# Optimization experiments

Measured on AMD Instinct MI355X. Metric: run time of the kernel, lower is better.

Reference implementation:

```python
import jax, jax.numpy as jnp
import numpy as np

B = 8
H1c = W1c = 56
H2c = W2c = 112
C1 = 512
C2 = 256
NH = 8
WS = 7
POOL = 2
EPS = 1e-5


def setup_inputs() -> dict:
    key = jax.random.key(0)
    ks = jax.random.split(key, 8)
    x = jax.random.normal(ks[0], (B, H1c * W1c, C1), dtype=jnp.float32)
    y = jax.random.normal(ks[1], (B, H2c * W2c, C2), dtype=jnp.float32)
    Wq = jax.random.normal(ks[2], (C1, C1), dtype=jnp.float32) * 0.02
    Wkv = jax.random.normal(ks[3], (2 * C1, C2), dtype=jnp.float32) * 0.02
    Wproj = jax.random.normal(ks[4], (C1, C1), dtype=jnp.float32) * 0.02
    bproj = jnp.zeros((C1,), dtype=jnp.float32)
    # 1x1 conv: fan_out = out_channels -> std = sqrt(2/C2)
    Wsr = jax.random.normal(ks[5], (C2, C2), dtype=jnp.float32) * np.sqrt(2.0 / C2).astype(np.float32)
    bsr = jnp.zeros((C2,), dtype=jnp.float32)
    gn = jnp.ones((C2,), dtype=jnp.float32)
    bn = jnp.zeros((C2,), dtype=jnp.float32)
    return {"x": x, "y": y, "Wq": Wq, "Wkv": Wkv, "Wproj": Wproj,
            "bproj": bproj, "Wsr": Wsr, "bsr": bsr, "gn": gn, "bn": bn,
            "H1": H1c, "W1": W1c, "H2": H2c, "W2": W2c}


def _window_partition(t, ws):
    # t: (B, nh, H, W, C) -> (B*nh, num_windows, ws*ws, C)
    Bt, n, H, W, C = t.shape
    ht, wt = H // ws, W // ws
    t = t.reshape(Bt, n, ht, ws, wt, ws, C).transpose(0, 1, 2, 4, 3, 5, 6)
    return t.reshape(Bt * n, ht * wt, ws * ws, C)


def reference(x, y, Wq, Wkv, Wproj, bproj, Wsr, bsr, gn, bn, H1, W1, H2, W2):
    B1, N1, c1 = x.shape
    B2, N2, c2 = y.shape
    nh, ws = NH, WS
    hd = c1 // nh
    scale = hd ** (-0.5)

    # q projection -> (B, nh, H1, W1, hd)
    q = (x @ Wq.T).reshape(B1, H1, W1, nh, hd).transpose(0, 3, 1, 2, 4)

    # KV preprocessing: avgpool -> 1x1 conv -> layernorm -> gelu
    y2 = y.transpose(0, 2, 1).reshape(B2, c2, H2, W2)
    Hp, Wp = H2 // POOL, W2 // POOL
    y2 = y2.reshape(B2, c2, Hp, POOL, Wp, POOL).mean(axis=(3, 5))
    y2 = jnp.einsum('bchw,oc->bohw', y2, Wsr) + bsr[None, :, None, None]
    y2 = y2.reshape(B2, c2, Hp * Wp).transpose(0, 2, 1)  # (B, Np, C2)
    mu = y2.mean(-1, keepdims=True)
    var = y2.var(-1, keepdims=True)
    y2 = (y2 - mu) / jnp.sqrt(var + EPS) * gn + bn
    y2 = jax.nn.gelu(y2, approximate=False)

    kv = (y2 @ Wkv.T).reshape(B2, Hp * Wp, 2, nh, hd)
    k = kv[:, :, 0].transpose(0, 2, 1, 3).reshape(B2, nh, Hp, Wp, hd)
    v = kv[:, :, 1].transpose(0, 2, 1, 3).reshape(B2, nh, Hp, Wp, hd)

    qw = _window_partition(q, ws)   # (B*nh, nw, ws^2, hd)
    kw = _window_partition(k, ws)
    vw = _window_partition(v, ws)

    attn = jax.nn.softmax(jnp.einsum('bnqd,bnkd->bnqk', qw, kw) * scale, axis=-1)
    out = jnp.einsum('bnqk,bnkd->bnqd', attn, vw)  # (B*nh, nw, ws^2, hd)

    # window reverse -> (B, N1, C1)
    ht, wt = H1 // ws, W1 // ws
    out = out.reshape(B1, nh, ht, wt, ws, ws, hd).transpose(0, 1, 2, 4, 3, 5, 6)
    out = out.reshape(B1, nh, H1 * W1, hd).transpose(0, 2, 1, 3).reshape(B1, H1 * W1, c1)
    return out @ Wproj.T + bproj
```

## Files before the change

kernel.cpp:

```cpp
#include <hip/hip_runtime.h>
#include <hip/hip_bf16.h>

typedef __attribute__((ext_vector_type(8))) short short8;
typedef __attribute__((ext_vector_type(4))) float f32x4;
typedef __attribute__((ext_vector_type(4))) unsigned short ushort4v;

#define DI __device__ __forceinline__

DI unsigned short f2bf(float f) {
  union { float f; unsigned int u; } a; a.f = f;
  unsigned int u = a.u;
  return (unsigned short)((u + 0x7FFFu + ((u >> 16) & 1u)) >> 16);
}

#define BARRIER() do { asm volatile("" ::: "memory"); __builtin_amdgcn_s_barrier(); asm volatile("" ::: "memory"); } while (0)
#define GLOAD16(src, dst) __builtin_amdgcn_global_load_lds( \
    (const __attribute__((address_space(1))) void*)(src), \
    (__attribute__((address_space(3))) void*)(dst), 16, 0, 0)


__global__ __launch_bounds__(256)
void cvt_pool(const float* __restrict__ y, unsigned short* __restrict__ pooled,
              const float* __restrict__ Wq, const float* __restrict__ Wsr,
              const float* __restrict__ Wkv, const float* __restrict__ Wproj,
              unsigned short* __restrict__ Wq_b, unsigned short* __restrict__ Wsr_b,
              unsigned short* __restrict__ WkvF, unsigned short* __restrict__ WprojF) {
  int bid = blockIdx.x;
  int tid = threadIdx.x;
  if (bid < 6272) {
    int t = bid * 256 + tid;
    int cv = (t & 63) * 4;
    int bp = t >> 6;
    int b = bp / 3136, p = bp % 3136;
    int hp = p / 56, wp = p % 56;
    const float* src = y + (((size_t)b * 12544) + hp * 224 + wp * 2) * 256 + cv;
    float4 a0 = *(const float4*)(src);
    float4 a1 = *(const float4*)(src + 256);
    float4 a2 = *(const float4*)(src + 28672);
    float4 a3 = *(const float4*)(src + 28672 + 256);
    float4 av;
    av.x = (a0.x + a1.x + a2.x + a3.x) * 0.25f;
    av.y = (a0.y + a1.y + a2.y + a3.y) * 0.25f;
    av.z = (a0.z + a1.z + a2.z + a3.z) * 0.25f;
    av.w = (a0.w + a1.w + a2.w + a3.w) * 0.25f;
    ushort4v o = { f2bf(av.x), f2bf(av.y), f2bf(av.z), f2bf(av.w) };
    *(ushort4v*)&pooled[(size_t)bp * 256 + cv] = o;
  } else if (bid < 6592) {
    const float* src; unsigned short* dst; long off;
    if (bid < 6528) { src = Wq;  dst = Wq_b;  off = (long)(bid - 6272) * 1024 + tid * 4; }
    else            { src = Wsr; dst = Wsr_b; off = (long)(bid - 6528) * 1024 + tid * 4; }
    float4 v = *(const float4*)&src[off];
    ushort4v o = { f2bf(v.x), f2bf(v.y), f2bf(v.z), f2bf(v.w) };
    *(ushort4v*)&dst[off] = o;
  } else if (bid < 6720) {
    int t = (bid - 6592) * 4 + (tid >> 6);
    int lane = tid & 63, lr = lane & 15, lg = lane >> 4;
    int ks = t & 1, kt = (t >> 1) & 3, nf2 = (t >> 3) & 1;
    int half = (t >> 4) & 1, head = (t >> 5) & 7, h2 = (t >> 8) & 1;
    int row = h2 * 512 + head * 64 + half * 32 + nf2 * 16 + lr;
    int col = kt * 64 + (ks * 4 + lg) * 8;
    const float* s = Wkv + (size_t)row * 256 + col;
    float4 v0 = *(const float4*)s, v1 = *(const float4*)(s + 4);
    union { short8 sv; unsigned short u[8]; } w;
    w.u[0] = f2bf(v0.x); w.u[1] = f2bf(v0.y); w.u[2] = f2bf(v0.z); w.u[3] = f2bf(v0.w);
    w.u[4] = f2bf(v1.x); w.u[5] = f2bf(v1.y); w.u[6] = f2bf(v1.z); w.u[7] = f2bf(v1.w);
    *(short8*)&WkvF[((size_t)t << 9) + lane * 8] = w.sv;
  } else {
    int t = (bid - 6720) * 4 + (tid >> 6);
    int lane = tid & 63, lr = lane & 15, lg = lane >> 4;
    int ks = t & 1, kt = (t >> 1) & 7, nf = (t >> 4) & 3, head = (t >> 6) & 7;
    int row = head * 64 + nf * 16 + lr;
    int col = kt * 64 + (ks * 4 + lg) * 8;
    const float* s = Wproj + (size_t)row * 512 + col;
    float4 v0 = *(const float4*)s, v1 = *(const float4*)(s + 4);
    union { short8 sv; unsigned short u[8]; } w;
    w.u[0] = f2bf(v0.x); w.u[1] = f2bf(v0.y); w.u[2] = f2bf(v0.z); w.u[3] = f2bf(v0.w);
    w.u[4] = f2bf(v1.x); w.u[5] = f2bf(v1.y); w.u[6] = f2bf(v1.z); w.u[7] = f2bf(v1.w);
    *(short8*)&WprojF[((size_t)t << 9) + lane * 8] = w.sv;
  }
}

__global__ __launch_bounds__(256)
void sr_gemm(const unsigned short* __restrict__ Ap, const unsigned short* __restrict__ Wsr_b,
             const float* __restrict__ bsr, const float* __restrict__ gn,
             const float* __restrict__ bn, unsigned short* __restrict__ out) {
  __shared__ unsigned short sA[64 * 64];
  __shared__ unsigned short sB[256 * 64];
  __shared__ float red[64 * 8];

  const int tid = threadIdx.x;
  const int wv = tid >> 6;
  const int lane = tid & 63;
  const int lr = lane & 15;
  const int lg = lane >> 4;
  const int lr4 = lg * 4;
  const int m0 = blockIdx.x * 64;
  const int sr8 = lane >> 3;
  const int sl8 = lane & 7;

  f32x4 acc[4][4];
#pragma unroll
  for (int i = 0; i < 4; ++i)
#pragma unroll
    for (int j = 0; j < 4; ++j) acc[i][j] = (f32x4){0.f, 0.f, 0.f, 0.f};

  for (int kt = 0; kt < 256; kt += 64) {
#pragma unroll
    for (int c = 0; c < 2; ++c) {
      int row = wv * 16 + c * 8 + sr8;
      GLOAD16(Ap + (size_t)(m0 + row) * 256 + kt + ((sl8 ^ (row & 7)) * 8),
              &sA[(wv * 16 + c * 8) * 64]);
    }
#pragma unroll
    for (int c = 0; c < 8; ++c) {
      int row = wv * 64 + c * 8 + sr8;
      GLOAD16(Wsr_b + (size_t)row * 256 + kt + ((sl8 ^ (row & 7)) * 8),
              &sB[(wv * 64 + c * 8) * 64]);
    }
    __syncthreads();
#pragma unroll
    for (int ks = 0; ks < 2; ++ks) {
      short8 af[4], bfr[4];
#pragma unroll
      for (int i = 0; i < 4; ++i)
        af[i] = *(const short8*)&sA[(i * 16 + lr) * 64 + (((ks * 4 + lg) ^ (lr & 7)) * 8)];
#pragma unroll
      for (int j = 0; j < 4; ++j)
        bfr[j] = *(const short8*)&sB[(wv * 64 + j * 16 + lr) * 64 + (((ks * 4 + lg) ^ (lr & 7)) * 8)];
#pragma unroll
      for (int i = 0; i < 4; ++i)
#pragma unroll
        for (int j = 0; j < 4; ++j)
          acc[i][j] = __builtin_amdgcn_mfma_f32_16x16x32_bf16(af[i], bfr[j], acc[i][j], 0, 0, 0);
    }
    __syncthreads();
  }

  float bsv[4], gnv[4], bnv[4];
#pragma unroll
  for (int j = 0; j < 4; ++j) {
    int col = wv * 64 + j * 16 + lr;
    bsv[j] = bsr[col]; gnv[j] = gn[col]; bnv[j] = bn[col];
  }
  float s_[4][4], q_[4][4];
#pragma unroll
  for (int i = 0; i < 4; ++i)
#pragma unroll
    for (int r = 0; r < 4; ++r) {
      float s = 0.f, q = 0.f;
#pragma unroll
      for (int j = 0; j < 4; ++j) {
        float v = acc[i][j][r] + bsv[j];
        acc[i][j][r] = v;
        s += v; q += v * v;
      }
      s_[i][r] = s; q_[i][r] = q;
    }
#pragma unroll
  for (int m = 1; m <= 8; m <<= 1)
#pragma unroll
    for (int i = 0; i < 4; ++i)
#pragma unroll
      for (int r = 0; r < 4; ++r) {
        s_[i][r] += __shfl_xor(s_[i][r], m);
        q_[i][r] += __shfl_xor(q_[i][r], m);
      }
  if (lr == 0) {
#pragma unroll
    for (int i = 0; i < 4; ++i)
#pragma unroll
      for (int r = 0; r < 4; ++r) {
        int row = i * 16 + lr4 + r;
        red[row * 8 + wv * 2 + 0] = s_[i][r];
        red[row * 8 + wv * 2 + 1] = q_[i][r];
      }
  }
  __syncthreads();
#pragma unroll
  for (int i = 0; i < 4; ++i) {
#pragma unroll
    for (int r = 0; r < 4; ++r) {
      int row = i * 16 + lr4 + r;
      float sum = red[row * 8 + 0] + red[row * 8 + 2] + red[row * 8 + 4] + red[row * 8 + 6];
      float sq  = red[row * 8 + 1] + red[row * 8 + 3] + red[row * 8 + 5] + red[row * 8 + 7];
      float mean = sum * (1.f / 256.f);
      float var = sq * (1.f / 256.f) - mean * mean;
      float rstd = rsqrtf(var + 1e-5f);
#pragma unroll
      for (int j = 0; j < 4; ++j) {
        float t = (acc[i][j][r] - mean) * rstd * gnv[j] + bnv[j];
        t = 0.5f * t * (1.f + erff(t * 0.70710678118654752f));
        out[(size_t)(m0 + row) * 256 + wv * 64 + j * 16 + lr] = f2bf(t);
      }
    }
  }
}

DI void epi_q(int gm, int gc, float v, unsigned short* outp) {
  const int b = gm / 3136, pos = gm % 3136;
  const int h = pos / 56, ww = pos % 56;
  const int head = gc >> 6, d = gc & 63;
  const size_t idx = ((((size_t)(b * 8 + head)) * 64 + (h / 7) * 8 + (ww / 7)) * 49
                      + (h % 7) * 7 + (ww % 7)) * 64 + d;
  outp[idx] = f2bf(v);
}

template<int K, int N>
__global__ __launch_bounds__(512, 2)
void gemm256f(const float* __restrict__ A,
              const unsigned short* __restrict__ Bw,
              unsigned short* __restrict__ outp) {
  __shared__ unsigned short lds[65536];
  const int tid = threadIdx.x;
  const int wv = tid >> 6;
  const int lane = tid & 63;
  const int wm = wv >> 2;
  const int wn = wv & 3;
  const int m0 = blockIdx.y * 256;
  const int n0 = blockIdx.x * 256;
  const int lr = lane & 15;
  const int lg = lane >> 4;
  const int lr4 = lg * 4;
  const int srow8 = lane >> 3;
  const int sl8 = lane & 7;
  constexpr int NT = K / 64;

  f32x4 acc[8][4];
#pragma unroll
  for (int i = 0; i < 8; ++i)
#pragma unroll
    for (int j = 0; j < 4; ++j) acc[i][j] = (f32x4){0.f, 0.f, 0.f, 0.f};

  float4 fa[4][2];
  auto loadA = [&](int t1) {
    int tsrc = (t1 < NT) ? t1 : NT - 1;
#pragma unroll
    for (int rr = 0; rr < 4; ++rr) {
      int trow = rr * 64 + wv * 8 + srow8;
      const float* p = A + (size_t)(m0 + trow) * K + tsrc * 64 + sl8 * 8;
      fa[rr][0] = *(const float4*)p;
      fa[rr][1] = *(const float4*)(p + 4);
    }
    asm volatile("" ::: "memory");
  };
  auto writeA = [&](int t1) {
#pragma unroll
    for (int rr = 0; rr < 4; ++rr) {
      int trow = rr * 64 + wv * 8 + srow8;
      union { short8 s; unsigned short u[8]; } w;
      w.u[0] = f2bf(fa[rr][0].x); w.u[1] = f2bf(fa[rr][0].y);
      w.u[2] = f2bf(fa[rr][0].z); w.u[3] = f2bf(fa[rr][0].w);
      w.u[4] = f2bf(fa[rr][1].x); w.u[5] = f2bf(fa[rr][1].y);
      w.u[6] = f2bf(fa[rr][1].z); w.u[7] = f2bf(fa[rr][1].w);
      *(short8*)&lds[(t1 & 1) * 32768 + trow * 64 + ((sl8 ^ (trow & 7)) * 8)] = w.s;
    }
  };
  auto stageB = [&](int t1, int rr) {
    int tsrc = (t1 < NT) ? t1 : NT - 1;
    int trow = rr * 64 + wv * 8 + srow8;
    int sx = sl8 ^ (trow & 7);
    GLOAD16(Bw + (size_t)(n0 + trow) * K + tsrc * 64 + sx * 8,
            &lds[(t1 & 1) * 32768 + 16384 + (rr * 64 + wv * 8) * 64]);
  };
  auto rdA = [&](int s, int mf, int ks) -> short8 {
    int row = wm * 128 + mf * 16 + lr;
    int slot = ((ks << 2) + lg) ^ (row & 7);
    return *(const short8*)&lds[s * 32768 + row * 64 + slot * 8];
  };
  auto rdB = [&](int s, int nf, int ks) -> short8 {
    int row = wn * 64 + nf * 16 + lr;
    int slot = ((ks << 2) + lg) ^ (row & 7);
    return *(const short8*)&lds[s * 32768 + 16384 + row * 64 + slot * 8];
  };

  stageB(0, 0); stageB(0, 1); stageB(0, 2); stageB(0, 3);
  loadA(0);
  asm volatile("s_waitcnt vmcnt(0)" ::: "memory");
  writeA(0);
  asm volatile("s_waitcnt lgkmcnt(0)" ::: "memory");
  BARRIER();

  for (int t = 0; t < NT; ++t) {
    const int s = t & 1;
    short8 bfr[4][2];
    loadA(t + 1);
#pragma unroll
    for (int j = 0; j < 4; ++j) { bfr[j][0] = rdB(s, j, 0); bfr[j][1] = rdB(s, j, 1); }
    {
      short8 x0 = rdA(s, 0, 0), x1 = rdA(s, 0, 1);
      short8 y0 = rdA(s, 1, 0), y1 = rdA(s, 1, 1);
      BARRIER();
      __builtin_amdgcn_s_setprio(1);
#pragma unroll
      for (int j = 0; j < 4; ++j) {
        acc[0][j] = __builtin_amdgcn_mfma_f32_16x16x32_bf16(x0, bfr[j][0], acc[0][j], 0, 0, 0);
        acc[0][j] = __builtin_amdgcn_mfma_f32_16x16x32_bf16(x1, bfr[j][1], acc[0][j], 0, 0, 0);
        acc[1][j] = __builtin_amdgcn_mfma_f32_16x16x32_bf16(y0, bfr[j][0], acc[1][j], 0, 0, 0);
        acc[1][j] = __builtin_amdgcn_mfma_f32_16x16x32_bf16(y1, bfr[j][1], acc[1][j], 0, 0, 0);
      }
      __builtin_amdgcn_s_setprio(0);
      BARRIER();
    }
    stageB(t + 1, 0); stageB(t + 1, 1);
    {
      short8 x0 = rdA(s, 2, 0), x1 = rdA(s, 2, 1);
      short8 y0 = rdA(s, 3, 0), y1 = rdA(s, 3, 1);
      BARRIER();
      __builtin_amdgcn_s_setprio(1);
#pragma unroll
      for (int j = 0; j < 4; ++j) {
        acc[2][j] = __builtin_amdgcn_mfma_f32_16x16x32_bf16(x0, bfr[j][0], acc[2][j], 0, 0, 0);
        acc[2][j] = __builtin_amdgcn_mfma_f32_16x16x32_bf16(x1, bfr[j][1], acc[2][j], 0, 0, 0);
        acc[3][j] = __builtin_amdgcn_mfma_f32_16x16x32_bf16(y0, bfr[j][0], acc[3][j], 0, 0, 0);
        acc[3][j] = __builtin_amdgcn_mfma_f32_16x16x32_bf16(y1, bfr[j][1], acc[3][j], 0, 0, 0);
      }
      __builtin_amdgcn_s_setprio(0);
      BARRIER();
    }
    stageB(t + 1, 2); stageB(t + 1, 3);
    {
      short8 x0 = rdA(s, 4, 0), x1 = rdA(s, 4, 1);
      short8 y0 = rdA(s, 5, 0), y1 = rdA(s, 5, 1);
      BARRIER();
      __builtin_amdgcn_s_setprio(1);
#pragma unroll
      for (int j = 0; j < 4; ++j) {
        acc[4][j] = __builtin_amdgcn_mfma_f32_16x16x32_bf16(x0, bfr[j][0], acc[4][j], 0, 0, 0);
        acc[4][j] = __builtin_amdgcn_mfma_f32_16x16x32_bf16(x1, bfr[j][1], acc[4][j], 0, 0, 0);
        acc[5][j] = __builtin_amdgcn_mfma_f32_16x16x32_bf16(y0, bfr[j][0], acc[5][j], 0, 0, 0);
        acc[5][j] = __builtin_amdgcn_mfma_f32_16x16x32_bf16(y1, bfr[j][1], acc[5][j], 0, 0, 0);
      }
      __builtin_amdgcn_s_setprio(0);
      BARRIER();
    }
    {
      short8 x0 = rdA(s, 6, 0), x1 = rdA(s, 6, 1);
      short8 y0 = rdA(s, 7, 0), y1 = rdA(s, 7, 1);
      asm volatile("s_waitcnt vmcnt(4)" ::: "memory");
      writeA(t + 1);
      asm volatile("s_waitcnt lgkmcnt(0)" ::: "memory");
      BARRIER();
      __builtin_amdgcn_s_setprio(1);
#pragma unroll
      for (int j = 0; j < 4; ++j) {
        acc[6][j] = __builtin_amdgcn_mfma_f32_16x16x32_bf16(x0, bfr[j][0], acc[6][j], 0, 0, 0);
        acc[6][j] = __builtin_amdgcn_mfma_f32_16x16x32_bf16(x1, bfr[j][1], acc[6][j], 0, 0, 0);
        acc[7][j] = __builtin_amdgcn_mfma_f32_16x16x32_bf16(y0, bfr[j][0], acc[7][j], 0, 0, 0);
        acc[7][j] = __builtin_amdgcn_mfma_f32_16x16x32_bf16(y1, bfr[j][1], acc[7][j], 0, 0, 0);
      }
      __builtin_amdgcn_s_setprio(0);
      asm volatile("s_waitcnt vmcnt(0)" ::: "memory");
      BARRIER();
    }
  }

#pragma unroll
  for (int i = 0; i < 8; ++i)
#pragma unroll
    for (int j = 0; j < 4; ++j)
#pragma unroll
      for (int r = 0; r < 4; ++r)
        epi_q(m0 + wm * 128 + i * 16 + lr4 + r, n0 + wn * 64 + j * 16 + lr,
              acc[i][j][r], outp);
}

__global__ __launch_bounds__(1024)
void kvattn(const unsigned short* __restrict__ y2,
            const unsigned short* __restrict__ WkvF,
            const unsigned short* __restrict__ qwin,
            const unsigned short* __restrict__ WprojF,
            const float* __restrict__ bproj,
            float* __restrict__ out) {
  __shared__ unsigned short lds[81920];
  const int tid = threadIdx.x;
  const int wv16 = tid >> 6;
  const int head = wv16 >> 1;
  const int half = wv16 & 1;
  const int lane = tid & 63;
  const int lr = lane & 15;
  const int lg = lane >> 4;
  const int r8 = lane >> 3;
  const int sl8 = lane & 7;
  const int bb = blockIdx.x >> 6;
  const int win = blockIdx.x & 63;
  const int ht = win >> 3, wt = win & 7;

  unsigned short* Cy  = lds;
  unsigned short* SLh = lds + 16384 + head * 8192;
  unsigned short* OA  = lds;

  {
    int rb = wv16 & 7;
    int m = rb * 8 + r8;
    int mm = (m < 49) ? m : 48;
    int grow = bb * 3136 + (ht * 7 + mm / 7) * 56 + wt * 7 + (mm % 7);
    int p0 = wv16 >> 3;
#pragma unroll
    for (int pp = 0; pp < 2; ++pp) {
      int panel = p0 + pp * 2;
      GLOAD16(y2 + (size_t)grow * 256 + panel * 64 + ((sl8 ^ (m & 7)) * 8),
              &Cy[panel * 4096 + rb * 512]);
    }
  }
  asm volatile("s_waitcnt vmcnt(0)" ::: "memory");
  BARRIER();

  f32x4 aK[4][2], aV[4][2];
#pragma unroll
  for (int i = 0; i < 4; ++i)
#pragma unroll
    for (int j = 0; j < 2; ++j) { aK[i][j] = (f32x4){0,0,0,0}; aV[i][j] = (f32x4){0,0,0,0}; }

  auto ldKV = [&](int s, short8* dst) {
    int kt = s >> 1, h2 = s & 1;
#pragma unroll
    for (int nf2 = 0; nf2 < 2; ++nf2)
#pragma unroll
      for (int ks = 0; ks < 2; ++ks) {
        int t = (h2 << 8) | (head << 5) | (half << 4) | (nf2 << 3) | (kt << 1) | ks;
        dst[nf2 * 2 + ks] = *(const short8*)&WkvF[((size_t)t << 9) + lane * 8];
      }
  };

  short8 cur[4], nxt[4];
  ldKV(0, cur);
  short8 af[4][2];
#pragma unroll
  for (int s = 0; s < 8; ++s) {
    if (s < 7) ldKV(s + 1, nxt);
    if ((s & 1) == 0) {
      int kt = s >> 1;
#pragma unroll
      for (int mf = 0; mf < 4; ++mf)
#pragma unroll
        for (int ks = 0; ks < 2; ++ks)
          af[mf][ks] = *(const short8*)&Cy[kt * 4096 + (mf * 16 + lr) * 64 + (((ks * 4 + lg) ^ (lr & 7)) * 8)];
    }
#pragma unroll
    for (int mf = 0; mf < 4; ++mf)
#pragma unroll
      for (int ks = 0; ks < 2; ++ks)
#pragma unroll
        for (int nf2 = 0; nf2 < 2; ++nf2) {
          if ((s & 1) == 0)
            aK[mf][nf2] = __builtin_amdgcn_mfma_f32_16x16x32_bf16(af[mf][ks], cur[nf2 * 2 + ks], aK[mf][nf2], 0, 0, 0);
          else
            aV[mf][nf2] = __builtin_amdgcn_mfma_f32_16x16x32_bf16(af[mf][ks], cur[nf2 * 2 + ks], aV[mf][nf2], 0, 0, 0);
        }
    if (s < 7) { cur[0] = nxt[0]; cur[1] = nxt[1]; cur[2] = nxt[2]; cur[3] = nxt[3]; }
  }

  const unsigned short* qb = qwin + (size_t)((bb * 8 + head) * 64 + win) * 3136;
  short8 qf[2][2];
#pragma unroll
  for (int mf2 = 0; mf2 < 2; ++mf2)
#pragma unroll
    for (int ks = 0; ks < 2; ++ks)
      qf[mf2][ks] = *(const short8*)&qb[((half * 2 + mf2) * 16 + lr) * 64 + ks * 32 + lg * 8];

#pragma unroll
  for (int mf = 0; mf < 4; ++mf)
#pragma unroll
    for (int nf2 = 0; nf2 < 2; ++nf2)
#pragma unroll
      for (int r = 0; r < 4; ++r) {
        int key = mf * 16 + lg * 4 + r;
        int d = (half * 2 + nf2) * 16 + lr;
        SLh[key * 64 + (((d >> 3) ^ (key & 7)) * 8) + (d & 7)] = f2bf(aK[mf][nf2][r]);
        SLh[4096 + d * 64 + (((key >> 3) ^ (d & 7)) * 8) + (key & 7)] = f2bf(aV[mf][nf2][r]);
      }
  asm volatile("s_waitcnt lgkmcnt(0)" ::: "memory");
  BARRIER();

  f32x4 aS[2][4];
#pragma unroll
  for (int i = 0; i < 2; ++i)
#pragma unroll
    for (int j = 0; j < 4; ++j) aS[i][j] = (f32x4){0,0,0,0};
#pragma unroll
  for (int mf2 = 0; mf2 < 2; ++mf2)
#pragma unroll
    for (int ks = 0; ks < 2; ++ks)
#pragma unroll
      for (int nf = 0; nf < 4; ++nf) {
        short8 bk = *(const short8*)&SLh[(nf * 16 + lr) * 64 + (((ks * 4 + lg) ^ (lr & 7)) * 8)];
        aS[mf2][nf] = __builtin_amdgcn_mfma_f32_16x16x32_bf16(qf[mf2][ks], bk, aS[mf2][nf], 0, 0, 0);
      }

#pragma unroll
  for (int nf = 0; nf < 4; ++nf)
    if (nf * 16 + lr >= 49) {
#pragma unroll
      for (int mf2 = 0; mf2 < 2; ++mf2)
#pragma unroll
        for (int r = 0; r < 4; ++r) aS[mf2][nf][r] = -1e30f;
    }
  const float cexp = 0.125f * 1.4426950408889634f;
  float mx[2][4], sm[2][4];
#pragma unroll
  for (int mf2 = 0; mf2 < 2; ++mf2)
#pragma unroll
    for (int r = 0; r < 4; ++r)
      mx[mf2][r] = fmaxf(fmaxf(aS[mf2][0][r], aS[mf2][1][r]), fmaxf(aS[mf2][2][r], aS[mf2][3][r]));
#pragma unroll
  for (int m = 1; m <= 8; m <<= 1)
#pragma unroll
    for (int mf2 = 0; mf2 < 2; ++mf2)
#pragma unroll
      for (int r = 0; r < 4; ++r) mx[mf2][r] = fmaxf(mx[mf2][r], __shfl_xor(mx[mf2][r], m));
#pragma unroll
  for (int mf2 = 0; mf2 < 2; ++mf2)
#pragma unroll
    for (int nf = 0; nf < 4; ++nf)
#pragma unroll
      for (int r = 0; r < 4; ++r)
        aS[mf2][nf][r] = exp2f((aS[mf2][nf][r] - mx[mf2][r]) * cexp);
#pragma unroll
  for (int mf2 = 0; mf2 < 2; ++mf2)
#pragma unroll
    for (int r = 0; r < 4; ++r)
      sm[mf2][r] = aS[mf2][0][r] + aS[mf2][1][r] + aS[mf2][2][r] + aS[mf2][3][r];
#pragma unroll
  for (int m = 1; m <= 8; m <<= 1)
#pragma unroll
    for (int mf2 = 0; mf2 < 2; ++mf2)
#pragma unroll
      for (int r = 0; r < 4; ++r) sm[mf2][r] += __shfl_xor(sm[mf2][r], m);
#pragma unroll
  for (int mf2 = 0; mf2 < 2; ++mf2)
#pragma unroll
    for (int r = 0; r < 4; ++r) sm[mf2][r] = 1.f / sm[mf2][r];

  BARRIER();

#pragma unroll
  for (int mf2 = 0; mf2 < 2; ++mf2)
#pragma unroll
    for (int nf = 0; nf < 4; ++nf)
#pragma unroll
      for (int r = 0; r < 4; ++r) {
        int q = (half * 2 + mf2) * 16 + lg * 4 + r;
        int key = nf * 16 + lr;
        SLh[q * 64 + (((key >> 3) ^ (q & 7)) * 8) + (key & 7)] = f2bf(aS[mf2][nf][r] * sm[mf2][r]);
      }

  f32x4 aO[2][4];
#pragma unroll
  for (int i = 0; i < 2; ++i)
#pragma unroll
    for (int j = 0; j < 4; ++j) aO[i][j] = (f32x4){0,0,0,0};
#pragma unroll
  for (int mf2 = 0; mf2 < 2; ++mf2)
#pragma unroll
    for (int ks = 0; ks < 2; ++ks) {
      int qrow = (half * 2 + mf2) * 16 + lr;
      short8 pf = *(const short8*)&SLh[qrow * 64 + (((ks * 4 + lg) ^ (lr & 7)) * 8)];
#pragma unroll
      for (int df = 0; df < 4; ++df) {
        short8 vf = *(const short8*)&SLh[4096 + (df * 16 + lr) * 64 + (((ks * 4 + lg) ^ (lr & 7)) * 8)];
        aO[mf2][df] = __builtin_amdgcn_mfma_f32_16x16x32_bf16(pf, vf, aO[mf2][df], 0, 0, 0);
      }
    }

  BARRIER();

#pragma unroll
  for (int mf2 = 0; mf2 < 2; ++mf2)
#pragma unroll
    for (int df = 0; df < 4; ++df)
#pragma unroll
      for (int r = 0; r < 4; ++r) {
        int q = (half * 2 + mf2) * 16 + lg * 4 + r;
        int slot = df * 2 + (lr >> 3);
        OA[q * 512 + head * 64 + ((slot ^ (q & 7)) * 8) + (lr & 7)] = f2bf(aO[mf2][df][r]);
      }
  asm volatile("s_waitcnt lgkmcnt(0)" ::: "memory");
  BARRIER();

  f32x4 aR[2][4];
#pragma unroll
  for (int i = 0; i < 2; ++i)
#pragma unroll
    for (int j = 0; j < 4; ++j) aR[i][j] = (f32x4){0,0,0,0};

  auto ldPj = [&](int u, short8* dst) {
    int kt = u >> 1, ks = u & 1;
#pragma unroll
    for (int nf = 0; nf < 4; ++nf) {
      int t = (head << 6) | (nf << 4) | (kt << 1) | ks;
      dst[nf] = *(const short8*)&WprojF[((size_t)t << 9) + lane * 8];
    }
  };
  short8 pc[4], pn[4];
  ldPj(0, pc);
#pragma unroll
  for (int u = 0; u < 16; ++u) {
    if (u < 15) ldPj(u + 1, pn);
    int kt = u >> 1, ks = u & 1;
    short8 a0 = *(const short8*)&OA[(half * 32 + lr) * 512 + kt * 64 + (((ks * 4 + lg) ^ (lr & 7)) * 8)];
    short8 a1 = *(const short8*)&OA[(half * 32 + 16 + lr) * 512 + kt * 64 + (((ks * 4 + lg) ^ (lr & 7)) * 8)];
#pragma unroll
    for (int nf = 0; nf < 4; ++nf) {
      aR[0][nf] = __builtin_amdgcn_mfma_f32_16x16x32_bf16(a0, pc[nf], aR[0][nf], 0, 0, 0);
      aR[1][nf] = __builtin_amdgcn_mfma_f32_16x16x32_bf16(a1, pc[nf], aR[1][nf], 0, 0, 0);
    }
    if (u < 15) { pc[0] = pn[0]; pc[1] = pn[1]; pc[2] = pn[2]; pc[3] = pn[3]; }
  }

#pragma unroll
  for (int mf = 0; mf < 2; ++mf)
#pragma unroll
    for (int nf = 0; nf < 4; ++nf)
#pragma unroll
      for (int r = 0; r < 4; ++r) {
        int q = half * 32 + mf * 16 + lg * 4 + r;
        if (q < 49) {
          int gm = bb * 3136 + (ht * 7 + q / 7) * 56 + wt * 7 + (q % 7);
          int col = head * 64 + nf * 16 + lr;
          out[(size_t)gm * 512 + col] = aR[mf][nf][r] + bproj[col];
        }
      }
}

extern "C" void kernel_launch(void* const* d_in, const int* in_sizes, int n_in,
                              void* d_out, int out_size, void* d_ws, size_t ws_size,
                              hipStream_t stream) {
  const float* x     = (const float*)d_in[0];
  const float* y     = (const float*)d_in[1];
  const float* Wq    = (const float*)d_in[2];
  const float* Wkv   = (const float*)d_in[3];
  const float* Wproj = (const float*)d_in[4];
  const float* bproj = (const float*)d_in[5];
  const float* Wsr   = (const float*)d_in[6];
  const float* bsr   = (const float*)d_in[7];
  const float* gn    = (const float*)d_in[8];
  const float* bn    = (const float*)d_in[9];
  float* out = (float*)d_out;

  char* ws = (char*)d_ws;
  unsigned short* Wq_b    = (unsigned short*)ws; ws += 524288;
  unsigned short* Wsr_b   = (unsigned short*)ws; ws += 131072;
  unsigned short* WkvF    = (unsigned short*)ws; ws += 524288;
  unsigned short* WprojF  = (unsigned short*)ws; ws += 524288;
  unsigned short* regA    = (unsigned short*)ws; ws += 12845056;
  unsigned short* q_win   = (unsigned short*)ws; ws += 25690112;
  unsigned short* regC    = (unsigned short*)ws; ws += 12845056;

  cvt_pool<<<6848, 256, 0, stream>>>(y, regA, Wq, Wsr, Wkv, Wproj,
                                     Wq_b, Wsr_b, WkvF, WprojF);

  gemm256f<512, 512><<<dim3(2, 98), 512, 0, stream>>>(x, Wq_b, q_win);

  sr_gemm<<<392, 256, 0, stream>>>(regA, Wsr_b, bsr, gn, bn, regC);

  kvattn<<<512, 1024, 0, stream>>>(regC, WkvF, q_win, WprojF, bproj, out);
}
```

Before: 163.1 us.

## Stage KV weights through LDS with double-buffered async loads in kvattn

Wkv is now converted to a plain row-major bf16 copy instead of a per-lane fragment layout. In kvattn each head's two waves cooperatively load it into a swizzled, double-buffered LDS region via global_load_lds and read MFMA B fragments from LDS, rather than each wave fetching its fragments straight from global memory into registers. The Wproj loop is also restructured to prefetch a full k-tile (8 fragments) at a time. This trades register-held prefetch for LDS traffic, plus an extra barrier and vmcnt waits per stage. It relies on the SLh region not overlapping Cy while in use.

```diff
diff --git a/kernel.cpp b/kernel.cpp
--- a/kernel.cpp
+++ b/kernel.cpp
@@ -24,7 +24,7 @@
               const float* __restrict__ Wq, const float* __restrict__ Wsr,
               const float* __restrict__ Wkv, const float* __restrict__ Wproj,
               unsigned short* __restrict__ Wq_b, unsigned short* __restrict__ Wsr_b,
-              unsigned short* __restrict__ WkvF, unsigned short* __restrict__ WprojF) {
+              unsigned short* __restrict__ Wkv_b, unsigned short* __restrict__ WprojF) {
   int bid = blockIdx.x;
   int tid = threadIdx.x;
   if (bid < 6272) {
@@ -45,28 +45,16 @@
     av.w = (a0.w + a1.w + a2.w + a3.w) * 0.25f;
     ushort4v o = { f2bf(av.x), f2bf(av.y), f2bf(av.z), f2bf(av.w) };
     *(ushort4v*)&pooled[(size_t)bp * 256 + cv] = o;
-  } else if (bid < 6592) {
+  } else if (bid < 6848) {
     const float* src; unsigned short* dst; long off;
-    if (bid < 6528) { src = Wq;  dst = Wq_b;  off = (long)(bid - 6272) * 1024 + tid * 4; }
-    else            { src = Wsr; dst = Wsr_b; off = (long)(bid - 6528) * 1024 + tid * 4; }
+    if (bid < 6528)      { src = Wq;  dst = Wq_b;  off = (long)(bid - 6272) * 1024 + tid * 4; }
+    else if (bid < 6592) { src = Wsr; dst = Wsr_b; off = (long)(bid - 6528) * 1024 + tid * 4; }
+    else                 { src = Wkv; dst = Wkv_b; off = (long)(bid - 6592) * 1024 + tid * 4; }
     float4 v = *(const float4*)&src[off];
     ushort4v o = { f2bf(v.x), f2bf(v.y), f2bf(v.z), f2bf(v.w) };
     *(ushort4v*)&dst[off] = o;
-  } else if (bid < 6720) {
-    int t = (bid - 6592) * 4 + (tid >> 6);
-    int lane = tid & 63, lr = lane & 15, lg = lane >> 4;
-    int ks = t & 1, kt = (t >> 1) & 3, nf2 = (t >> 3) & 1;
-    int half = (t >> 4) & 1, head = (t >> 5) & 7, h2 = (t >> 8) & 1;
-    int row = h2 * 512 + head * 64 + half * 32 + nf2 * 16 + lr;
-    int col = kt * 64 + (ks * 4 + lg) * 8;
-    const float* s = Wkv + (size_t)row * 256 + col;
-    float4 v0 = *(const float4*)s, v1 = *(const float4*)(s + 4);
-    union { short8 sv; unsigned short u[8]; } w;
-    w.u[0] = f2bf(v0.x); w.u[1] = f2bf(v0.y); w.u[2] = f2bf(v0.z); w.u[3] = f2bf(v0.w);
-    w.u[4] = f2bf(v1.x); w.u[5] = f2bf(v1.y); w.u[6] = f2bf(v1.z); w.u[7] = f2bf(v1.w);
-    *(short8*)&WkvF[((size_t)t << 9) + lane * 8] = w.sv;
   } else {
-    int t = (bid - 6720) * 4 + (tid >> 6);
+    int t = (bid - 6848) * 4 + (tid >> 6);
     int lane = tid & 63, lr = lane & 15, lg = lane >> 4;
     int ks = t & 1, kt = (t >> 1) & 7, nf = (t >> 4) & 3, head = (t >> 6) & 7;
     int row = head * 64 + nf * 16 + lr;
@@ -366,7 +354,7 @@
 
 __global__ __launch_bounds__(1024)
 void kvattn(const unsigned short* __restrict__ y2,
-            const unsigned short* __restrict__ WkvF,
+            const unsigned short* __restrict__ Wkv_b,
             const unsigned short* __restrict__ qwin,
             const unsigned short* __restrict__ WprojF,
             const float* __restrict__ bproj,
@@ -402,34 +390,47 @@
               &Cy[panel * 4096 + rb * 512]);
     }
   }
-  asm volatile("s_waitcnt vmcnt(0)" ::: "memory");
+
+  auto stageW = [&](int s) {
+    int kt = s >> 1, h2 = s & 1;
+#pragma unroll
+    for (int c = 0; c < 4; ++c) {
+      int lrow = half * 32 + c * 8 + r8;
+      GLOAD16(Wkv_b + (size_t)(h2 * 512 + head * 64 + lrow) * 256 + kt * 64 + ((sl8 ^ r8) * 8),
+              &SLh[(s & 1) * 4096 + (half * 32 + c * 8) * 64]);
+    }
+  };
+
+  f32x4 aK[4][2], aV[4][2];
+#pragma unroll
+  for (int i = 0; i < 4; ++i)
+#pragma unroll
+    for (int j = 0; j < 2; ++j) { aK[i][j] = (f32x4){0,0,0,0}; aV[i][j] = (f32x4){0,0,0,0}; }
+
+  stageW(0);
+  asm volatile("s_waitcnt vmcnt(4)" ::: "memory");
   BARRIER();
 
-  f32x4 aK[4][2], aV[4][2];
-#pragma unroll
-  for (int i = 0; i < 4; ++i)
-#pragma unroll
-    for (int j = 0; j < 2; ++j) { aK[i][j] = (f32x4){0,0,0,0}; aV[i][j] = (f32x4){0,0,0,0}; }
-
-  auto ldKV = [&](int s, short8* dst) {
-    int kt = s >> 1, h2 = s & 1;
+  short8 af[4][2];
+#pragma unroll
+  for (int s = 0; s < 8; ++s) {
+    if (s < 7) {
+      stageW(s + 1);
+      asm volatile("s_waitcnt vmcnt(4)" ::: "memory");
+    } else {
+      asm volatile("s_waitcnt vmcnt(0)" ::: "memory");
+    }
+    const int kt = s >> 1;
+    const unsigned short* Wb = &SLh[(s & 1) * 4096];
+    short8 bfrg[2][2];
 #pragma unroll
     for (int nf2 = 0; nf2 < 2; ++nf2)
 #pragma unroll
       for (int ks = 0; ks < 2; ++ks) {
-        int t = (h2 << 8) | (head << 5) | (half << 4) | (nf2 << 3) | (kt << 1) | ks;
-        dst[nf2 * 2 + ks] = *(const short8*)&WkvF[((size_t)t << 9) + lane * 8];
-      }
-  };
-
-  short8 cur[4], nxt[4];
-  ldKV(0, cur);
-  short8 af[4][2];
-#pragma unroll
-  for (int s = 0; s < 8; ++s) {
-    if (s < 7) ldKV(s + 1, nxt);
+        int row = (half * 2 + nf2) * 16 + lr;
+        bfrg[nf2][ks] = *(const short8*)&Wb[row * 64 + (((ks * 4 + lg) ^ (lr & 7)) * 8)];
+      }
     if ((s & 1) == 0) {
-      int kt = s >> 1;
 #pragma unroll
       for (int mf = 0; mf < 4; ++mf)
 #pragma unroll
@@ -443,11 +444,10 @@
 #pragma unroll
         for (int nf2 = 0; nf2 < 2; ++nf2) {
           if ((s & 1) == 0)
-            aK[mf][nf2] = __builtin_amdgcn_mfma_f32_16x16x32_bf16(af[mf][ks], cur[nf2 * 2 + ks], aK[mf][nf2], 0, 0, 0);
+            aK[mf][nf2] = __builtin_amdgcn_mfma_f32_16x16x32_bf16(af[mf][ks], bfrg[nf2][ks], aK[mf][nf2], 0, 0, 0);
           else
-            aV[mf][nf2] = __builtin_amdgcn_mfma_f32_16x16x32_bf16(af[mf][ks], cur[nf2 * 2 + ks], aV[mf][nf2], 0, 0, 0);
+            aV[mf][nf2] = __builtin_amdgcn_mfma_f32_16x16x32_bf16(af[mf][ks], bfrg[nf2][ks], aV[mf][nf2], 0, 0, 0);
         }
-    if (s < 7) { cur[0] = nxt[0]; cur[1] = nxt[1]; cur[2] = nxt[2]; cur[3] = nxt[3]; }
   }
 
   const unsigned short* qb = qwin + (size_t)((bb * 8 + head) * 64 + win) * 3136;
@@ -457,6 +457,8 @@
 #pragma unroll
     for (int ks = 0; ks < 2; ++ks)
       qf[mf2][ks] = *(const short8*)&qb[((half * 2 + mf2) * 16 + lr) * 64 + ks * 32 + lg * 8];
+
+  BARRIER();
 
 #pragma unroll
   for (int mf = 0; mf < 4; ++mf)
@@ -583,28 +585,34 @@
 #pragma unroll
     for (int j = 0; j < 4; ++j) aR[i][j] = (f32x4){0,0,0,0};
 
-  auto ldPj = [&](int u, short8* dst) {
-    int kt = u >> 1, ks = u & 1;
-#pragma unroll
-    for (int nf = 0; nf < 4; ++nf) {
-      int t = (head << 6) | (nf << 4) | (kt << 1) | ks;
-      dst[nf] = *(const short8*)&WprojF[((size_t)t << 9) + lane * 8];
-    }
+  auto ldPj = [&](int kt, short8* dst) {
+#pragma unroll
+    for (int nf = 0; nf < 4; ++nf)
+#pragma unroll
+      for (int ks = 0; ks < 2; ++ks) {
+        int t = (head << 6) | (nf << 4) | (kt << 1) | ks;
+        dst[nf * 2 + ks] = *(const short8*)&WprojF[((size_t)t << 9) + lane * 8];
+      }
   };
-  short8 pc[4], pn[4];
+  short8 pc[8], pn[8];
   ldPj(0, pc);
 #pragma unroll
-  for (int u = 0; u < 16; ++u) {
-    if (u < 15) ldPj(u + 1, pn);
-    int kt = u >> 1, ks = u & 1;
-    short8 a0 = *(const short8*)&OA[(half * 32 + lr) * 512 + kt * 64 + (((ks * 4 + lg) ^ (lr & 7)) * 8)];
-    short8 a1 = *(const short8*)&OA[(half * 32 + 16 + lr) * 512 + kt * 64 + (((ks * 4 + lg) ^ (lr & 7)) * 8)];
-#pragma unroll
-    for (int nf = 0; nf < 4; ++nf) {
-      aR[0][nf] = __builtin_amdgcn_mfma_f32_16x16x32_bf16(a0, pc[nf], aR[0][nf], 0, 0, 0);
-      aR[1][nf] = __builtin_amdgcn_mfma_f32_16x16x32_bf16(a1, pc[nf], aR[1][nf], 0, 0, 0);
-    }
-    if (u < 15) { pc[0] = pn[0]; pc[1] = pn[1]; pc[2] = pn[2]; pc[3] = pn[3]; }
+  for (int kt = 0; kt < 8; ++kt) {
+    if (kt < 7) ldPj(kt + 1, pn);
+#pragma unroll
+    for (int ks = 0; ks < 2; ++ks) {
+      short8 a0 = *(const short8*)&OA[(half * 32 + lr) * 512 + kt * 64 + (((ks * 4 + lg) ^ (lr & 7)) * 8)];
+      short8 a1 = *(const short8*)&OA[(half * 32 + 16 + lr) * 512 + kt * 64 + (((ks * 4 + lg) ^ (lr & 7)) * 8)];
+#pragma unroll
+      for (int nf = 0; nf < 4; ++nf) {
+        aR[0][nf] = __builtin_amdgcn_mfma_f32_16x16x32_bf16(a0, pc[nf * 2 + ks], aR[0][nf], 0, 0, 0);
+        aR[1][nf] = __builtin_amdgcn_mfma_f32_16x16x32_bf16(a1, pc[nf * 2 + ks], aR[1][nf], 0, 0, 0);
+      }
+    }
+    if (kt < 7) {
+#pragma unroll
+      for (int e = 0; e < 8; ++e) pc[e] = pn[e];
+    }
   }
 
 #pragma unroll
@@ -640,18 +648,18 @@
   char* ws = (char*)d_ws;
   unsigned short* Wq_b    = (unsigned short*)ws; ws += 524288;
   unsigned short* Wsr_b   = (unsigned short*)ws; ws += 131072;
-  unsigned short* WkvF    = (unsigned short*)ws; ws += 524288;
+  unsigned short* Wkv_b   = (unsigned short*)ws; ws += 524288;
   unsigned short* WprojF  = (unsigned short*)ws; ws += 524288;
   unsigned short* regA    = (unsigned short*)ws; ws += 12845056;
   unsigned short* q_win   = (unsigned short*)ws; ws += 25690112;
   unsigned short* regC    = (unsigned short*)ws; ws += 12845056;
 
-  cvt_pool<<<6848, 256, 0, stream>>>(y, regA, Wq, Wsr, Wkv, Wproj,
-                                     Wq_b, Wsr_b, WkvF, WprojF);
+  cvt_pool<<<6976, 256, 0, stream>>>(y, regA, Wq, Wsr, Wkv, Wproj,
+                                     Wq_b, Wsr_b, Wkv_b, WprojF);
 
   gemm256f<512, 512><<<dim3(2, 98), 512, 0, stream>>>(x, Wq_b, q_win);
 
   sr_gemm<<<392, 256, 0, stream>>>(regA, Wsr_b, bsr, gn, bn, regC);
 
-  kvattn<<<512, 1024, 0, stream>>>(regC, WkvF, q_win, WprojF, bproj, out);
+  kvattn<<<512, 1024, 0, stream>>>(regC, Wkv_b, q_win, WprojF, bproj, out);
 }
```

Result: slower. 172.9 us (+6.0%).
